# Optimization experiments

Hardware: AMD Instinct MI355X
Metric: run time of the kernel (lower is better)

Reference implementation:

```python
import jax, jax.numpy as jnp
import numpy as np


def setup_inputs() -> dict:
    key = jax.random.key(0)
    ks = jax.random.split(key, 7)
    B, C, W, H = 4, 128, 64, 64
    Cq = C // 8
    x = jax.random.normal(ks[0], (B, C, W, H), jnp.float32)
    wq = jax.random.normal(ks[1], (Cq, C), jnp.float32) * 0.05
    bq = jax.random.normal(ks[2], (Cq,), jnp.float32) * 0.05
    wk = jax.random.normal(ks[3], (Cq, C), jnp.float32) * 0.05
    bk = jax.random.normal(ks[4], (Cq,), jnp.float32) * 0.05
    wv = jax.random.normal(ks[5], (C, C), jnp.float32) * 0.05
    bv = jax.random.normal(ks[6], (C,), jnp.float32) * 0.05
    gamma = jnp.ones((1,), jnp.float32)
    return {"x": x, "wq": wq, "bq": bq, "wk": wk, "bk": bk,
            "wv": wv, "bv": bv, "gamma": gamma}


def reference(x, wq, bq, wk, bk, wv, bv, gamma):
    B, C, W, H = x.shape
    N = W * H
    xf = x.reshape(B, C, N)  # flatten spatial dims (W fastest over H, as torch .view)
    # 1x1 convs == per-position linear maps
    q = jnp.einsum('dc,bcn->bnd', wq, xf) + bq            # [B, N, C//8]
    k = jnp.einsum('dc,bcn->bdn', wk, xf) + bk[:, None]   # [B, C//8, N]
    v = jnp.einsum('dc,bcn->bdn', wv, xf) + bv[:, None]   # [B, C, N]
    energy = jnp.einsum('bnd,bdm->bnm', q, k)             # [B, N, N]
    # block-causal mask: position i may attend only to j < (i//W + 1)*W
    i = jnp.arange(N)
    j = jnp.arange(N)
    masked = j[None, :] >= ((i[:, None] // W) + 1) * W    # True -> -inf
    energy = jnp.where(masked[None, :, :], -jnp.inf, energy)
    attention = jax.nn.softmax(energy, axis=-1)           # [B, N, N]
    # out[b,c,n] = sum_m V[b,c,m] * attn[b,n,m]  (torch bmm(V, attn^T))
    out = jnp.einsum('bcm,bnm->bcn', v, attention).reshape(B, C, W, H)
    out = gamma * out + x
    return (out, attention)
```

## Files before the change

### kernel.cpp

```cpp
#include <hip/hip_runtime.h>
#include <hip/hip_bf16.h>


typedef __attribute__((ext_vector_type(8))) short short8;
typedef __attribute__((ext_vector_type(16))) float float16;
typedef __attribute__((ext_vector_type(4))) float floatx4;

__device__ __forceinline__ ushort f2bf(float f) {
  union { float f; uint u; } v; v.f = f;
  return (ushort)((v.u + 0x7FFFu + ((v.u >> 16) & 1u)) >> 16);
}

#define LDS_BARRIER()                                             \
  do {                                                            \
    __builtin_amdgcn_sched_barrier(0);                            \
    asm volatile("s_waitcnt lgkmcnt(0)" ::: "memory");            \
    __builtin_amdgcn_sched_barrier(0);                            \
    __builtin_amdgcn_s_barrier();                                 \
    __builtin_amdgcn_sched_barrier(0);                            \
  } while (0)

__global__ __launch_bounds__(512, 2) void qkv_kernel(
    const float* __restrict__ x,
    const float* __restrict__ wq, const float* __restrict__ bq,
    const float* __restrict__ wk, const float* __restrict__ bk,
    const float* __restrict__ wv, const float* __restrict__ bv,
    ushort* __restrict__ qT, ushort* __restrict__ kT, ushort* __restrict__ vo) {
  __shared__ float xs[128 * 64];
  const int nt = blockIdx.x, b = blockIdx.y;
  const int n0 = nt * 64;
  const float* xb = x + (size_t)b * 524288 + n0;
  for (int idx = threadIdx.x; idx < 8192; idx += 512) {
    int c = idx >> 6, n = idx & 63;
    xs[idx] = xb[(size_t)c * 4096 + n];
  }
  __syncthreads();
  const int n = threadIdx.x & 63;
  const int og = __builtin_amdgcn_readfirstlane((int)(threadIdx.x >> 6));
  float acc[20];
#pragma unroll
  for (int i = 0; i < 20; i++) {
    int o = og + 8 * i;
    acc[i] = (i < 2) ? bq[o] : (i < 4) ? bk[o - 16] : bv[o - 32];
  }
#pragma unroll 4
  for (int c = 0; c < 128; c++) {
    float xr = xs[c * 64 + n];
#pragma unroll
    for (int i = 0; i < 20; i++) {
      int o = og + 8 * i;
      const float* wr = (i < 2) ? (wq + o * 128)
                      : (i < 4) ? (wk + (o - 16) * 128)
                                : (wv + (o - 32) * 128);
      acc[i] += wr[c] * xr;
    }
  }
  const size_t pos = (size_t)b * 4096 + n0 + n;
#pragma unroll
  for (int i = 0; i < 20; i++) {
    int o = og + 8 * i;
    if (i < 2)      qT[pos * 16 + o]      = f2bf(acc[i]);
    else if (i < 4) kT[pos * 16 + o - 16] = f2bf(acc[i]);
    else vo[(size_t)b * 524288 + (size_t)(o - 32) * 4096 + n0 + n] = f2bf(acc[i]);
  }
}

__global__ __launch_bounds__(512, 4) void fused_attn_kernel(
    const ushort* __restrict__ qT, const ushort* __restrict__ kT,
    const ushort* __restrict__ vws, const float* __restrict__ x,
    const float* __restrict__ g,
    float* __restrict__ attn, float* __restrict__ out) {
  __shared__ __align__(16) ushort Pt[8][32 * 72];
  __shared__ __align__(16) float red[32][8];
  const int bx = blockIdx.x;
  const int b = bx & 3;
  const int v_ = bx >> 2;
  const int half = v_ & 1;
  const int u = v_ >> 1;
  const int rb = (u < 32) ? u : 95 - u;
  const int S = rb + 1;
  const int lane = threadIdx.x & 63;
  const int w = __builtin_amdgcn_readfirstlane((int)(threadIdx.x >> 6));
  const int q = w & 3;
  const int hh = w >> 2;
  const int nblk = rb * 64 + half * 32;
  const int l31 = lane & 31;
  const int h = lane >> 5;
  const int hk = h * 8;
  const ushort* qb = qT + (size_t)b * 65536;
  const ushort* kb = kT + (size_t)b * 65536;
  const ushort* vp = vws + (size_t)b * 524288;
  float* ab = attn + (size_t)b * 16777216;

  const short8 qa = *(const short8*)(qb + (size_t)(nblk + l31) * 16 + hk);

  float16 zero16;
#pragma unroll
  for (int i = 0; i < 16; i++) zero16[i] = 0.f;

  float sume[16];
#pragma unroll
  for (int i = 0; i < 16; i++) sume[i] = 0.f;
  for (int s = w; s < S; s += 8) {
    const int m0 = s * 64;
#pragma unroll
    for (int mh = 0; mh < 2; mh++) {
      short8 kf = *(const short8*)(kb + (size_t)(m0 + mh * 32 + l31) * 16 + hk);
      float16 e = __builtin_amdgcn_mfma_f32_32x32x16_bf16(qa, kf, zero16, 0, 0, 0);
#pragma unroll
      for (int r = 0; r < 16; r++) sume[r] += __expf(e[r]);
    }
  }
#pragma unroll
  for (int r = 0; r < 16; r++) {
#pragma unroll
    for (int off = 1; off <= 16; off <<= 1)
      sume[r] += __shfl_xor(sume[r], off, 64);
  }
  if (l31 == 0) {
#pragma unroll
    for (int r = 0; r < 16; r++) {
      int row = (r & 3) + 8 * (r >> 2) + 4 * h;
      red[row][w] = sume[r];
    }
  }
  __syncthreads();
  float inv[16];
#pragma unroll
  for (int r = 0; r < 16; r++) {
    int row = (r & 3) + 8 * (r >> 2) + 4 * h;
    const float* pr = &red[row][0];
    float t = ((pr[0] + pr[1]) + (pr[2] + pr[3])) +
              ((pr[4] + pr[5]) + (pr[6] + pr[7]));
    inv[r] = 1.0f / t;
  }

  float16 acc = zero16;
  for (int s0 = 0; s0 < S; s0 += 8) {
    const int sl = (S - s0 < 8) ? (S - s0) : 8;
    if (w < sl) {
      const int m0 = (s0 + w) * 64;
      ushort* Pb = &Pt[w][0];
#pragma unroll
      for (int mh = 0; mh < 2; mh++) {
        short8 kf = *(const short8*)(kb + (size_t)(m0 + mh * 32 + l31) * 16 + hk);
        float16 e = __builtin_amdgcn_mfma_f32_32x32x16_bf16(qa, kf, zero16, 0, 0, 0);
#pragma unroll
        for (int r = 0; r < 16; r++) {
          int row = (r & 3) + 8 * (r >> 2) + 4 * h;
          float p = __expf(e[r]) * inv[r];
          ab[(size_t)(nblk + row) * 4096 + m0 + mh * 32 + l31] = p;
          Pb[row * 72 + mh * 32 + l31] = f2bf(p);
        }
      }
    }
    LDS_BARRIER();
    for (int ss = hh; ss < sl; ss += 2) {
      const int m0 = (s0 + ss) * 64;
      const ushort* vrow = vp + (size_t)(q * 32 + l31) * 4096 + m0 + hk;
      const ushort* Pr = &Pt[ss][l31 * 72 + hk];
#pragma unroll
      for (int kk = 0; kk < 4; kk++) {
        short8 a  = *(const short8*)(vrow + kk * 16);
        short8 bf = *(const short8*)(Pr + kk * 16);
        acc = __builtin_amdgcn_mfma_f32_32x32x16_bf16(a, bf, acc, 0, 0, 0);
      }
    }
    LDS_BARRIER();
  }

  float* accx = (float*)&Pt[0][0];
  if (hh == 1) {
#pragma unroll
    for (int reg = 0; reg < 16; reg++)
      accx[reg * 256 + q * 64 + lane] = acc[reg];
  }
  __syncthreads();
  if (hh == 0) {
#pragma unroll
    for (int reg = 0; reg < 16; reg++)
      acc[reg] += accx[reg * 256 + q * 64 + lane];
  }

  if (hh == 0) {
    const float gamma = g[0];
#pragma unroll
    for (int reg = 0; reg < 16; reg++) {
      int row = (reg & 3) + 8 * (reg >> 2) + 4 * h;
      int c = q * 32 + row;
      int n = nblk + l31;
      size_t off = (size_t)b * 524288 + (size_t)c * 4096 + n;
      out[off] = gamma * acc[reg] + x[off];
    }
  }
}

extern "C" void kernel_launch(void* const* d_in, const int* in_sizes, int n_in,
                              void* d_out, int out_size, void* d_ws, size_t ws_size,
                              hipStream_t stream) {
  const float* x  = (const float*)d_in[0];
  const float* wq = (const float*)d_in[1];
  const float* bq = (const float*)d_in[2];
  const float* wk = (const float*)d_in[3];
  const float* bk = (const float*)d_in[4];
  const float* wv = (const float*)d_in[5];
  const float* bv = (const float*)d_in[6];
  const float* gm = (const float*)d_in[7];
  float* out  = (float*)d_out;
  float* attn = out + 2097152;
  ushort* qTw = (ushort*)d_ws;
  ushort* kTw = qTw + 262144;
  ushort* vws = qTw + 524288;

  hipMemsetAsync(attn, 0, (size_t)268435456, stream);
  qkv_kernel<<<dim3(64, 4), 512, 0, stream>>>(x, wq, bq, wk, bk, wv, bv, qTw, kTw, vws);
  fused_attn_kernel<<<dim3(512), 512, 0, stream>>>(qTw, kTw, vws, x, gm, attn, out);
}
```

Measured before the change: 371.2 us.

## Make softmax single-pass with deferred normalization and in-kernel zero fill

Drops the separate row-sum pass that recomputed QK^T and exp. Unnormalized exponentials are now written to the attention output and fed to the PV MFMA while the row sums accumulate. The PV result is scaled by the inverse row sum at the end, and each block then rescales its attention rows in place. The same blocks zero-fill the masked tail of each row, which replaces the full-buffer hipMemsetAsync. This trades the recompute and the memset for an extra read-modify-write over the unmasked attention region, and the bf16 P operand now holds unnormalized values.

```diff
diff --git a/kernel.cpp b/kernel.cpp
--- a/kernel.cpp
+++ b/kernel.cpp
@@ -72,12 +72,13 @@
     float* __restrict__ attn, float* __restrict__ out) {
   __shared__ __align__(16) ushort Pt[8][32 * 72];
   __shared__ __align__(16) float red[32][8];
+  __shared__ __align__(16) float rsum[32];
   const int bx = blockIdx.x;
   const int b = bx & 3;
   const int v_ = bx >> 2;
   const int half = v_ & 1;
-  const int u = v_ >> 1;
-  const int rb = (u < 32) ? u : 95 - u;
+  const int u_ = v_ >> 1;
+  const int rb = (u_ < 32) ? u_ : 95 - u_;
   const int S = rb + 1;
   const int lane = threadIdx.x & 63;
   const int w = __builtin_amdgcn_readfirstlane((int)(threadIdx.x >> 6));
@@ -101,40 +102,6 @@
   float sume[16];
 #pragma unroll
   for (int i = 0; i < 16; i++) sume[i] = 0.f;
-  for (int s = w; s < S; s += 8) {
-    const int m0 = s * 64;
-#pragma unroll
-    for (int mh = 0; mh < 2; mh++) {
-      short8 kf = *(const short8*)(kb + (size_t)(m0 + mh * 32 + l31) * 16 + hk);
-      float16 e = __builtin_amdgcn_mfma_f32_32x32x16_bf16(qa, kf, zero16, 0, 0, 0);
-#pragma unroll
-      for (int r = 0; r < 16; r++) sume[r] += __expf(e[r]);
-    }
-  }
-#pragma unroll
-  for (int r = 0; r < 16; r++) {
-#pragma unroll
-    for (int off = 1; off <= 16; off <<= 1)
-      sume[r] += __shfl_xor(sume[r], off, 64);
-  }
-  if (l31 == 0) {
-#pragma unroll
-    for (int r = 0; r < 16; r++) {
-      int row = (r & 3) + 8 * (r >> 2) + 4 * h;
-      red[row][w] = sume[r];
-    }
-  }
-  __syncthreads();
-  float inv[16];
-#pragma unroll
-  for (int r = 0; r < 16; r++) {
-    int row = (r & 3) + 8 * (r >> 2) + 4 * h;
-    const float* pr = &red[row][0];
-    float t = ((pr[0] + pr[1]) + (pr[2] + pr[3])) +
-              ((pr[4] + pr[5]) + (pr[6] + pr[7]));
-    inv[r] = 1.0f / t;
-  }
-
   float16 acc = zero16;
   for (int s0 = 0; s0 < S; s0 += 8) {
     const int sl = (S - s0 < 8) ? (S - s0) : 8;
@@ -148,9 +115,10 @@
 #pragma unroll
         for (int r = 0; r < 16; r++) {
           int row = (r & 3) + 8 * (r >> 2) + 4 * h;
-          float p = __expf(e[r]) * inv[r];
-          ab[(size_t)(nblk + row) * 4096 + m0 + mh * 32 + l31] = p;
-          Pb[row * 72 + mh * 32 + l31] = f2bf(p);
+          float uu = __expf(e[r]);
+          sume[r] += uu;
+          ab[(size_t)(nblk + row) * 4096 + m0 + mh * 32 + l31] = uu;
+          Pb[row * 72 + mh * 32 + l31] = f2bf(uu);
         }
       }
     }
@@ -169,6 +137,19 @@
     LDS_BARRIER();
   }
 
+#pragma unroll
+  for (int r = 0; r < 16; r++) {
+#pragma unroll
+    for (int off = 1; off <= 16; off <<= 1)
+      sume[r] += __shfl_xor(sume[r], off, 64);
+  }
+  if (l31 == 0) {
+#pragma unroll
+    for (int r = 0; r < 16; r++) {
+      int row = (r & 3) + 8 * (r >> 2) + 4 * h;
+      red[row][w] = sume[r];
+    }
+  }
   float* accx = (float*)&Pt[0][0];
   if (hh == 1) {
 #pragma unroll
@@ -176,22 +157,41 @@
       accx[reg * 256 + q * 64 + lane] = acc[reg];
   }
   __syncthreads();
-  if (hh == 0) {
-#pragma unroll
-    for (int reg = 0; reg < 16; reg++)
-      acc[reg] += accx[reg * 256 + q * 64 + lane];
-  }
+  if (w == 0 && lane < 32) {
+    const float* pr = &red[lane][0];
+    rsum[lane] = ((pr[0] + pr[1]) + (pr[2] + pr[3])) +
+                 ((pr[4] + pr[5]) + (pr[6] + pr[7]));
+  }
+  __syncthreads();
 
   if (hh == 0) {
     const float gamma = g[0];
+    const float invc = 1.0f / rsum[l31];
 #pragma unroll
     for (int reg = 0; reg < 16; reg++) {
       int row = (reg & 3) + 8 * (reg >> 2) + 4 * h;
+      float at = acc[reg] + accx[reg * 256 + q * 64 + lane];
       int c = q * 32 + row;
       int n = nblk + l31;
       size_t off = (size_t)b * 524288 + (size_t)c * 4096 + n;
-      out[off] = gamma * acc[reg] + x[off];
-    }
+      out[off] = gamma * (at * invc) + x[off];
+    }
+  }
+
+  const int M = S * 64;
+  const int M4 = M >> 2;
+  const floatx4 z = {0.f, 0.f, 0.f, 0.f};
+#pragma unroll
+  for (int rr = 0; rr < 4; rr++) {
+    const int row = w * 4 + rr;
+    const float invr = 1.0f / rsum[row];
+    floatx4* rowp = (floatx4*)(ab + (size_t)(nblk + row) * 4096);
+    for (int i4 = lane; i4 < M4; i4 += 64) {
+      floatx4 v = rowp[i4];
+      v *= invr;
+      rowp[i4] = v;
+    }
+    for (int i4 = M4 + lane; i4 < 1024; i4 += 64) rowp[i4] = z;
   }
 }
 
@@ -212,7 +212,6 @@
   ushort* kTw = qTw + 262144;
   ushort* vws = qTw + 524288;
 
-  hipMemsetAsync(attn, 0, (size_t)268435456, stream);
   qkv_kernel<<<dim3(64, 4), 512, 0, stream>>>(x, wq, bq, wk, bk, wv, bv, qTw, kTw, vws);
   fused_attn_kernel<<<dim3(512), 512, 0, stream>>>(qTw, kTw, vws, x, gm, attn, out);
 }
```

Result: slower. 387.3 us (+4.3%).
